# Performance work log

Measured on AMD Instinct MI355X. Metric: run time of the kernel, lower is better.

## Reference

```python
import jax, jax.numpy as jnp
import numpy as np

EMBED_DIM = 1024
NUM_HEADS = 16
SEQ_LEN = 2048
BATCH = 2
LN_EPS = 1e-5


def setup_inputs() -> dict:
    key = jax.random.key(0)
    ks = jax.random.split(key, 12)
    d = EMBED_DIM
    s = 1.0 / np.sqrt(d)
    inp = {
        "x": jax.random.normal(ks[0], (BATCH, SEQ_LEN, d), dtype=jnp.float32),
        "ln1_g": jnp.ones((d,), jnp.float32),
        "ln1_b": jnp.zeros((d,), jnp.float32),
        "ln2_g": jnp.ones((d,), jnp.float32),
        "ln2_b": jnp.zeros((d,), jnp.float32),
        "W_qkv": jax.random.normal(ks[1], (d, 3 * d), jnp.float32) * s,
        "b_qkv": jnp.zeros((3 * d,), jnp.float32),
        "W_proj": jax.random.normal(ks[2], (d, d), jnp.float32) * s,
        "b_proj": jnp.zeros((d,), jnp.float32),
        "W_fc": jax.random.normal(ks[3], (d, 4 * d), jnp.float32) * s,
        "b_fc": jnp.zeros((4 * d,), jnp.float32),
        "W_out": jax.random.normal(ks[4], (4 * d, d), jnpp_dummy := jnp.float32) * (1.0 / np.sqrt(4 * d)),
        "b_out": jnp.zeros((d,), jnp.float32),
    }
    return inp


def _layernorm(x, g, b):
    mu = jnp.mean(x, axis=-1, keepdims=True)
    var = jnp.mean(jnp.square(x - mu), axis=-1, keepdims=True)
    return (x - mu) * jax.lax.rsqrt(var + LN_EPS) * g + b


def _block(x, ln1_g, ln1_b, ln2_g, ln2_b, W_qkv, b_qkv, W_proj, b_proj, W_fc, b_fc, W_out, b_out):
    B, S, D = x.shape
    H = NUM_HEADS
    hd = D // H
    h = _layernorm(x, ln1_g, ln1_b)
    qkv = h @ W_qkv + b_qkv  # [B,S,3D]
    q, k, v = jnp.split(qkv, 3, axis=-1)
    # [B,H,S,hd]
    q = q.reshape(B, S, H, hd).transpose(0, 2, 1, 3)
    k = k.reshape(B, S, H, hd).transpose(0, 2, 1, 3)
    v = v.reshape(B, S, H, hd).transpose(0, 2, 1, 3)
    attn = jnp.einsum("bhqd,bhkd->bhqk", q, k) / np.sqrt(hd).astype(np.float32)
    causal = jnp.tril(jnp.ones((S, S), dtype=bool))
    attn = jnp.where(causal, attn, -jnp.inf)
    attn = jax.nn.softmax(attn, axis=-1)
    y = jnp.einsum("bhqk,bhkd->bhqd", attn, v)
    y = y.transpose(0, 2, 1, 3).reshape(B, S, D)
    y = y @ W_proj + b_proj
    x = x + y
    h2 = _layernorm(x, ln2_g, ln2_b)
    m = jax.nn.relu(h2 @ W_fc + b_fc) @ W_out + b_out
    return x + m


def reference(x, ln1_g, ln1_b, ln2_g, ln2_b, W_qkv, b_qkv, W_proj, b_proj, W_fc, b_fc, W_out, b_out):
    return _block(x, ln1_g, ln1_b, ln2_g, ln2_b, W_qkv, b_qkv, W_proj, b_proj, W_fc, b_fc, W_out, b_out)
```

## Files before the change

kernel.cpp:

```cpp
#include <hip/hip_runtime.h>

typedef unsigned short u16;
typedef __attribute__((ext_vector_type(8))) __bf16 bf16x8;
typedef __attribute__((ext_vector_type(4))) float f32x4;

#define DEV __device__ __forceinline__

DEV u16 f2bf(float f) {
  unsigned u = __float_as_uint(f);
  u += 0x7fffu + ((u >> 16) & 1u);
  return (u16)(u >> 16);
}
DEV float bf2f(u16 u) { return __uint_as_float((unsigned)u << 16); }

DEV void gl_lds16(const void* g, void* l) {
  __builtin_amdgcn_global_load_lds(
      (const __attribute__((address_space(1))) void*)(uintptr_t)g,
      (__attribute__((address_space(3))) void*)(unsigned)(uintptr_t)l, 16, 0, 0);
}

DEV float wave_sum64(float v) {
#pragma unroll
  for (int off = 32; off > 0; off >>= 1) v += __shfl_down(v, off);
  return v;
}

DEV void ln_body(const float4 v, const float* g, const float* be, u16* out_row, int t,
                 float* red) {
  const int w = t >> 6, L = t & 63;
  float s = v.x + v.y + v.z + v.w;
  s = wave_sum64(s);
  if (L == 0) red[w] = s;
  __syncthreads();
  const float mean = (red[0] + red[1] + red[2] + red[3]) * (1.0f / 1024.0f);
  const float dx = v.x - mean, dy = v.y - mean, dz = v.z - mean, dw = v.w - mean;
  float q = dx * dx + dy * dy + dz * dz + dw * dw;
  q = wave_sum64(q);
  if (L == 0) red[4 + w] = q;
  __syncthreads();
  const float var = (red[4] + red[5] + red[6] + red[7]) * (1.0f / 1024.0f);
  const float rs = rsqrtf(var + 1e-5f);
  const float4 gg = reinterpret_cast<const float4*>(g)[t];
  const float4 bb = reinterpret_cast<const float4*>(be)[t];
  ushort4 o;
  o.x = f2bf(dx * rs * gg.x + bb.x);
  o.y = f2bf(dy * rs * gg.y + bb.y);
  o.z = f2bf(dz * rs * gg.z + bb.z);
  o.w = f2bf(dw * rs * gg.w + bb.w);
  reinterpret_cast<ushort4*>(out_row)[t] = o;
}

__global__ __launch_bounds__(256) void prep_kernel(
    const float* __restrict__ x, const float* __restrict__ ln1g,
    const float* __restrict__ ln1b, u16* __restrict__ hbuf,
    const float* __restrict__ Wqkv, u16* __restrict__ wt_qkv,
    const float* __restrict__ Wproj, u16* __restrict__ wt_proj,
    const float* __restrict__ Wfc, u16* __restrict__ wt_fc,
    const float* __restrict__ Wout, u16* __restrict__ wt_out) {
  __shared__ float smem[32 * 33];
  int id = blockIdx.x;
  const int t = threadIdx.x;
  if (id < 4096) {
    const float4 v = reinterpret_cast<const float4*>(x + (size_t)id * 1024)[t];
    ln_body(v, ln1g, ln1b, hbuf + (size_t)id * 1024, t, smem);
    return;
  }
  id -= 4096;
  const float* W;
  u16* Wt;
  int K, N, nbx;
  if (id < 3072) {
    W = Wqkv; Wt = wt_qkv; K = 1024; N = 3072; nbx = 96;
  } else if (id < 3072 + 1024) {
    id -= 3072; W = Wproj; Wt = wt_proj; K = 1024; N = 1024; nbx = 32;
  } else if (id < 3072 + 1024 + 4096) {
    id -= 3072 + 1024; W = Wfc; Wt = wt_fc; K = 1024; N = 4096; nbx = 128;
  } else {
    id -= 3072 + 1024 + 4096; W = Wout; Wt = wt_out; K = 4096; N = 1024; nbx = 32;
  }
  float(*tile)[33] = (float(*)[33])smem;
  const int c0 = (id % nbx) * 32, r0 = (id / nbx) * 32;
  const int tx = t & 31, ty = t >> 5;
#pragma unroll
  for (int j = 0; j < 4; ++j)
    tile[ty + j * 8][tx] = W[(size_t)(r0 + ty + j * 8) * N + c0 + tx];
  __syncthreads();
#pragma unroll
  for (int j = 0; j < 4; ++j) {
    const int n = c0 + ty + j * 8, k = r0 + tx;
    Wt[(size_t)n * K + k] = f2bf(tile[tx][ty + j * 8]);
  }
}

__global__ __launch_bounds__(256) void proj_reduce_ln(const float* __restrict__ x,
                                                      const float* __restrict__ bias,
                                                      const u16* __restrict__ P0,
                                                      const u16* __restrict__ P1,
                                                      const float* __restrict__ g,
                                                      const float* __restrict__ be,
                                                      float* __restrict__ x2,
                                                      u16* __restrict__ hbuf) {
  const int row = blockIdx.x, t = threadIdx.x;
  const size_t off = (size_t)row * 1024;
  __shared__ float red[8];
  const float4 xv = reinterpret_cast<const float4*>(x + off)[t];
  const float4 bv = reinterpret_cast<const float4*>(bias)[t];
  const ushort4 p0 = reinterpret_cast<const ushort4*>(P0 + off)[t];
  const ushort4 p1 = reinterpret_cast<const ushort4*>(P1 + off)[t];
  float4 v;
  v.x = xv.x + bv.x + bf2f(p0.x) + bf2f(p1.x);
  v.y = xv.y + bv.y + bf2f(p0.y) + bf2f(p1.y);
  v.z = xv.z + bv.z + bf2f(p0.z) + bf2f(p1.z);
  v.w = xv.w + bv.w + bf2f(p0.w) + bf2f(p1.w);
  reinterpret_cast<float4*>(x2 + off)[t] = v;
  ln_body(v, g, be, hbuf + off, t, red);
}

__global__ __launch_bounds__(256) void out_reduce(const float* __restrict__ x2,
                                                  const float* __restrict__ bias,
                                                  const u16* __restrict__ P0,
                                                  const u16* __restrict__ P1,
                                                  const u16* __restrict__ P2,
                                                  const u16* __restrict__ P3,
                                                  float* __restrict__ dout) {
  const int row = blockIdx.x, t = threadIdx.x;
  const size_t off = (size_t)row * 1024;
  const float4 xv = reinterpret_cast<const float4*>(x2 + off)[t];
  const float4 bv = reinterpret_cast<const float4*>(bias)[t];
  const ushort4 a = reinterpret_cast<const ushort4*>(P0 + off)[t];
  const ushort4 b = reinterpret_cast<const ushort4*>(P1 + off)[t];
  const ushort4 c = reinterpret_cast<const ushort4*>(P2 + off)[t];
  const ushort4 d = reinterpret_cast<const ushort4*>(P3 + off)[t];
  float4 o;
  o.x = xv.x + bv.x + bf2f(a.x) + bf2f(b.x) + bf2f(c.x) + bf2f(d.x);
  o.y = xv.y + bv.y + bf2f(a.y) + bf2f(b.y) + bf2f(c.y) + bf2f(d.y);
  o.z = xv.z + bv.z + bf2f(a.z) + bf2f(b.z) + bf2f(c.z) + bf2f(d.z);
  o.w = xv.w + bv.w + bf2f(a.w) + bf2f(b.w) + bf2f(c.w) + bf2f(d.w);
  reinterpret_cast<float4*>(dout + off)[t] = o;
}

enum { F_BIAS = 1, F_RESID = 2, F_RELU = 4, F_BF16 = 8, F_PART4 = 32, F_VT = 64 };

template <int FLAGS>
__global__ __launch_bounds__(256, 2) void gemm_bt(const u16* __restrict__ A,
                                                  const u16* __restrict__ Bt,
                                                  const float* __restrict__ bias,
                                                  const float* __restrict__ resid,
                                                  void* __restrict__ Cout,
                                                  u16* __restrict__ pp0, u16* __restrict__ pp1,
                                                  u16* __restrict__ pp2, u16* __restrict__ pp3,
                                                  int M, int N, int K, int Kst) {
  __shared__ __attribute__((aligned(16))) u16 sA[2][128 * 32];
  __shared__ __attribute__((aligned(16))) u16 sB[2][128 * 32];

  const int gx = gridDim.x, gy = gridDim.y;
  const int tilesPerZ = gx * gy;
  int lin = (blockIdx.z * gy + blockIdx.y) * gx + blockIdx.x;
  const int total = tilesPerZ * gridDim.z;
  if (!(total & 7)) lin = (lin & 7) * (total >> 3) + (lin >> 3);
  const int zz = lin / tilesPerZ;
  const int pid = lin - zz * tilesPerZ;
  const int npg = gx << 3;
  const int gid = pid / npg;
  const int rem = pid - gid * npg;
  const int fm = gid << 3;
  const int gsm = (gy - fm < 8) ? (gy - fm) : 8;
  const int bm = fm + rem % gsm;
  const int bn = rem / gsm;

  const int t = threadIdx.x, w = t >> 6, L = t & 63, quad = L >> 4, l15 = L & 15;
  const int wm = w >> 1, wn = w & 1;
  const int m0 = bm * 128, n0 = bn * 128;
  const u16* Ag = A + (size_t)m0 * Kst + (size_t)zz * K;
  const u16* Bg = Bt + (size_t)n0 * Kst + (size_t)zz * K;

  f32x4 acc[4][4] = {};

  for (int k0 = 0; k0 < K; k0 += 64) {
    __syncthreads();
#pragma unroll
    for (int h = 0; h < 2; ++h) {
#pragma unroll
      for (int i = 0; i < 2; ++i) {
        const int cp = i * 256 + t, rr = cp >> 2, cc = (cp & 3) << 3;
        gl_lds16(Ag + (size_t)rr * Kst + k0 + h * 32 + cc, &sA[h][(i * 256 + w * 64) * 8]);
      }
#pragma unroll
      for (int i = 0; i < 2; ++i) {
        const int cp = i * 256 + t, rr = cp >> 2, cc = (cp & 3) << 3;
        gl_lds16(Bg + (size_t)rr * Kst + k0 + h * 32 + cc, &sB[h][(i * 256 + w * 64) * 8]);
      }
    }
    __syncthreads();

#pragma unroll
    for (int h = 0; h < 2; ++h) {
      bf16x8 af[4], bfr[4];
#pragma unroll
      for (int m = 0; m < 4; ++m)
        af[m] = *(const bf16x8*)&sA[h][(wm * 64 + m * 16 + l15) * 32 + quad * 8];
#pragma unroll
      for (int n = 0; n < 4; ++n)
        bfr[n] = *(const bf16x8*)&sB[h][(wn * 64 + n * 16 + l15) * 32 + quad * 8];
#pragma unroll
      for (int m = 0; m < 4; ++m)
#pragma unroll
        for (int n = 0; n < 4; ++n)
          acc[m][n] =
              __builtin_amdgcn_mfma_f32_16x16x32_bf16(af[m], bfr[n], acc[m][n], 0, 0, 0);
    }
  }

  if ((FLAGS & F_VT) && n0 >= 2048) {
#pragma unroll
    for (int m = 0; m < 4; ++m) {
#pragma unroll
      for (int n = 0; n < 4; ++n) {
        const int col = n0 + wn * 64 + n * 16 + l15;
        const float bv = bias[col];
        const int hh = (col - 2048) >> 6, dd = col & 63;
        const int srow = m0 + wm * 64 + m * 16 + quad * 4;
        const int bb = srow >> 11, ss = srow & 2047;
        ushort4 tmp;
        tmp.x = f2bf(acc[m][n][0] + bv);
        tmp.y = f2bf(acc[m][n][1] + bv);
        tmp.z = f2bf(acc[m][n][2] + bv);
        tmp.w = f2bf(acc[m][n][3] + bv);
        *(ushort4*)(pp0 + ((size_t)((bb * 16 + hh) * 64 + dd)) * 2048 + ss) = tmp;
      }
    }
    return;
  }

  u16* pbase = nullptr;
  if (FLAGS & F_PART4)
    pbase = (zz == 0) ? pp0 : (zz == 1) ? pp1 : (zz == 2) ? pp2 : pp3;

#pragma unroll
  for (int m = 0; m < 4; ++m) {
#pragma unroll
    for (int n = 0; n < 4; ++n) {
      const int col = n0 + wn * 64 + n * 16 + l15;
      const float bv = (FLAGS & F_BIAS) ? bias[col] : 0.0f;
#pragma unroll
      for (int rr = 0; rr < 4; ++rr) {
        const int row = m0 + wm * 64 + m * 16 + quad * 4 + rr;
        if (FLAGS & F_PART4) {
          pbase[(size_t)row * N + col] = f2bf(acc[m][n][rr]);
        } else {
          float v = acc[m][n][rr] + bv;
          if (FLAGS & F_RESID) v += resid[(size_t)row * N + col];
          if (FLAGS & F_RELU) v = fmaxf(v, 0.0f);
          if (FLAGS & F_BF16)
            ((u16*)Cout)[(size_t)row * N + col] = f2bf(v);
          else
            ((float*)Cout)[(size_t)row * N + col] = v;
        }
      }
    }
  }
}

__global__ __launch_bounds__(256) void flash_attn(const u16* __restrict__ qkv,
                                                  const u16* __restrict__ Vt,
                                                  u16* __restrict__ y) {
  constexpr int S = 2048, D3 = 3072, D = 1024;
  constexpr float Csc = 0.125f * 1.44269504088896f;
  __shared__ __attribute__((aligned(16))) u16 sK[2 * 64 * 32];
  __shared__ __attribute__((aligned(16))) u16 sV[2 * 64 * 32];
  __shared__ __attribute__((aligned(16))) u16 sP[4][2 * 16 * 40];

  const int lin = blockIdx.x;
  const int half = lin >> 9, rem = lin & 511;
  const int qt = half ? (31 - (rem & 31)) : (rem & 31);
  const int bh = (rem >> 5) | (half << 4);
  const int b = bh >> 4, h = bh & 15;
  const int q0 = qt * 64;

  const int t = threadIdx.x, w = t >> 6, L = t & 63, quad = L >> 4, l15 = L & 15;
  const int qw = q0 + w * 16;

  const u16* qbase = qkv + (size_t)(b * S) * D3 + h * 64;
  const u16* Kbase = qbase + D;
  const u16* Vbase = Vt + (size_t)((b * 16 + h) * 64) * S;

  bf16x8 aQ[2];
#pragma unroll
  for (int kk = 0; kk < 2; ++kk)
    aQ[kk] = *(const bf16x8*)(qbase + (size_t)(qw + l15) * D3 + kk * 32 + quad * 8);

  bf16x8 ones;
#pragma unroll
  for (int i = 0; i < 8; ++i) ones[i] = (__bf16)1.0f;

  f32x4 acc[4] = {};
  f32x4 lacc = {};

  u16* sPw = sP[w];
  const int nkv = qt + 1;
  for (int it = 0; it < nkv; ++it) {
    const int kv0 = it * 64;
    __syncthreads();
#pragma unroll
    for (int i = 0; i < 2; ++i) {
      const int cp = i * 256 + t;
      const int kk = cp >> 8, r = (cp >> 2) & 63, col = (cp & 3) << 3;
      gl_lds16(Kbase + (size_t)(kv0 + r) * D3 + kk * 32 + col, &sK[(i * 256 + w * 64) * 8]);
    }
#pragma unroll
    for (int i = 0; i < 2; ++i) {
      const int cp = i * 256 + t;
      const int kk = cp >> 8, d = (cp >> 2) & 63, col = (cp & 3) << 3;
      gl_lds16(Vbase + (size_t)d * S + kv0 + kk * 32 + col, &sV[(i * 256 + w * 64) * 8]);
    }
    __syncthreads();

    f32x4 s[4] = {};
#pragma unroll
    for (int kk = 0; kk < 2; ++kk) {
#pragma unroll
      for (int n = 0; n < 4; ++n) {
        const bf16x8 bK = *(const bf16x8*)&sK[kk * 2048 + (n * 16 + l15) * 32 + quad * 8];
        s[n] = __builtin_amdgcn_mfma_f32_16x16x32_bf16(aQ[kk], bK, s[n], 0, 0, 0);
      }
    }

    if (kv0 + 63 > qw) {
#pragma unroll
      for (int n = 0; n < 4; ++n) {
        const int col = kv0 + n * 16 + l15;
#pragma unroll
        for (int r = 0; r < 4; ++r) {
          const int row = qw + quad * 4 + r;
          const float p = __builtin_amdgcn_exp2f(s[n][r] * Csc);
          s[n][r] = (col > row) ? 0.0f : p;
        }
      }
    } else {
#pragma unroll
      for (int n = 0; n < 4; ++n)
#pragma unroll
        for (int r = 0; r < 4; ++r) s[n][r] = __builtin_amdgcn_exp2f(s[n][r] * Csc);
    }

#pragma unroll
    for (int n = 0; n < 4; ++n)
#pragma unroll
      for (int r = 0; r < 4; ++r)
        sPw[(n >> 1) * 640 + (quad * 4 + r) * 40 + (n & 1) * 16 + l15] = f2bf(s[n][r]);

#pragma unroll
    for (int kk = 0; kk < 2; ++kk) {
      const bf16x8 aP = *(const bf16x8*)&sPw[kk * 640 + l15 * 40 + quad * 8];
      lacc = __builtin_amdgcn_mfma_f32_16x16x32_bf16(aP, ones, lacc, 0, 0, 0);
#pragma unroll
      for (int dn = 0; dn < 4; ++dn) {
        const bf16x8 bV = *(const bf16x8*)&sV[kk * 2048 + (dn * 16 + l15) * 32 + quad * 8];
        acc[dn] = __builtin_amdgcn_mfma_f32_16x16x32_bf16(aP, bV, acc[dn], 0, 0, 0);
      }
    }
  }

#pragma unroll
  for (int r = 0; r < 4; ++r) {
    const float inv = 1.0f / lacc[r];
    const int row = qw + quad * 4 + r;
    u16* yb = y + (size_t)(b * S + row) * D + h * 64 + l15;
#pragma unroll
    for (int dn = 0; dn < 4; ++dn) yb[dn * 16] = f2bf(acc[dn][r] * inv);
  }
}

extern "C" void kernel_launch(void* const* d_in, const int* in_sizes, int n_in,
                              void* d_out, int out_size, void* d_ws, size_t ws_size,
                              hipStream_t stream) {
  const float* x = (const float*)d_in[0];
  const float* ln1g = (const float*)d_in[1];
  const float* ln1b = (const float*)d_in[2];
  const float* ln2g = (const float*)d_in[3];
  const float* ln2b = (const float*)d_in[4];
  const float* Wqkv = (const float*)d_in[5];
  const float* bqkv = (const float*)d_in[6];
  const float* Wproj = (const float*)d_in[7];
  const float* bproj = (const float*)d_in[8];
  const float* Wfc = (const float*)d_in[9];
  const float* bfc = (const float*)d_in[10];
  const float* Wout = (const float*)d_in[11];
  const float* bout = (const float*)d_in[12];

  char* ws = (char*)d_ws;
  const size_t MB = 1u << 20;
  u16* wt_out = (u16*)(ws + 0 * MB);
  u16* hbuf = (u16*)(ws + 8 * MB);
  float* x2 = (float*)(ws + 16 * MB);
  u16* ybuf = (u16*)(ws + 32 * MB);
  u16* qkvb = (u16*)(ws + 40 * MB);
  u16* vtb = (u16*)(ws + 64 * MB);
  u16* wt_qkv = (u16*)(ws + 72 * MB);
  u16* wt_proj = (u16*)(ws + 78 * MB);
  u16* wt_fc = (u16*)(ws + 80 * MB);
  u16* projP0 = (u16*)(ws + 40 * MB);
  u16* projP1 = (u16*)(ws + 48 * MB);
  u16* m1 = (u16*)(ws + 40 * MB);
  u16* po0 = (u16*)(ws + 8 * MB);
  u16* po1 = (u16*)(ws + 32 * MB);
  u16* po2 = (u16*)(ws + 72 * MB);
  u16* po3 = (u16*)(ws + 80 * MB);

  prep_kernel<<<4096 + 3072 + 1024 + 4096 + 4096, 256, 0, stream>>>(
      x, ln1g, ln1b, hbuf, Wqkv, wt_qkv, Wproj, wt_proj, Wfc, wt_fc, Wout, wt_out);

  gemm_bt<F_BIAS | F_BF16 | F_VT><<<dim3(24, 32), 256, 0, stream>>>(
      hbuf, wt_qkv, bqkv, nullptr, qkvb, vtb, nullptr, nullptr, nullptr,
      4096, 3072, 1024, 1024);
  flash_attn<<<1024, 256, 0, stream>>>(qkvb, vtb, ybuf);

  gemm_bt<F_PART4><<<dim3(8, 32, 2), 256, 0, stream>>>(
      ybuf, wt_proj, nullptr, nullptr, nullptr, projP0, projP1, nullptr, nullptr,
      4096, 1024, 512, 1024);
  proj_reduce_ln<<<4096, 256, 0, stream>>>(x, bproj, projP0, projP1, ln2g, ln2b, x2, hbuf);

  gemm_bt<F_BIAS | F_RELU | F_BF16><<<dim3(32, 32), 256, 0, stream>>>(
      hbuf, wt_fc, bfc, nullptr, m1, nullptr, nullptr, nullptr, nullptr,
      4096, 4096, 1024, 1024);

  gemm_bt<F_PART4><<<dim3(8, 32, 4), 256, 0, stream>>>(
      m1, wt_out, nullptr, nullptr, nullptr, po0, po1, po2, po3,
      4096, 1024, 1024, 4096);
  out_reduce<<<4096, 256, 0, stream>>>(x2, bout, po0, po1, po2, po3, (float*)d_out);
}
```

Measured before the change: 320.8 us.

## Double-buffer K/V tiles in flash attention with XOR-swizzled LDS layout

```diff
diff --git a/kernel.cpp b/kernel.cpp
--- a/kernel.cpp
+++ b/kernel.cpp
@@ -266,8 +266,8 @@
                                                   u16* __restrict__ y) {
   constexpr int S = 2048, D3 = 3072, D = 1024;
   constexpr float Csc = 0.125f * 1.44269504088896f;
-  __shared__ __attribute__((aligned(16))) u16 sK[2 * 64 * 32];
-  __shared__ __attribute__((aligned(16))) u16 sV[2 * 64 * 32];
+  __shared__ __attribute__((aligned(16))) u16 sK[2][64 * 64];
+  __shared__ __attribute__((aligned(16))) u16 sV[2][64 * 64];
   __shared__ __attribute__((aligned(16))) u16 sP[4][2 * 16 * 40];
 
   const int lin = blockIdx.x;
@@ -284,6 +284,17 @@
   const u16* Kbase = qbase + D;
   const u16* Vbase = Vt + (size_t)((b * 16 + h) * 64) * S;
 
+  const u16* Ksrc[2];
+  const u16* Vsrc[2];
+#pragma unroll
+  for (int i = 0; i < 2; ++i) {
+    const int p = i * 256 + t;
+    const int row = p >> 3;
+    const int k8 = ((p & 7) ^ (row & 7)) << 3;
+    Ksrc[i] = Kbase + (size_t)row * D3 + k8;
+    Vsrc[i] = Vbase + (size_t)row * S + k8;
+  }
+
   bf16x8 aQ[2];
 #pragma unroll
   for (int kk = 0; kk < 2; ++kk)
@@ -297,30 +308,43 @@
   f32x4 lacc = {};
 
   u16* sPw = sP[w];
+  const int swz = l15 & 7;
   const int nkv = qt + 1;
+
+#pragma unroll
+  for (int i = 0; i < 2; ++i)
+    gl_lds16(Ksrc[i], &sK[0][(i * 256 + w * 64) * 8]);
+#pragma unroll
+  for (int i = 0; i < 2; ++i)
+    gl_lds16(Vsrc[i], &sV[0][(i * 256 + w * 64) * 8]);
+
+  int cur = 0;
   for (int it = 0; it < nkv; ++it) {
     const int kv0 = it * 64;
-    __syncthreads();
-#pragma unroll
-    for (int i = 0; i < 2; ++i) {
-      const int cp = i * 256 + t;
-      const int kk = cp >> 8, r = (cp >> 2) & 63, col = (cp & 3) << 3;
-      gl_lds16(Kbase + (size_t)(kv0 + r) * D3 + kk * 32 + col, &sK[(i * 256 + w * 64) * 8]);
-    }
-#pragma unroll
-    for (int i = 0; i < 2; ++i) {
-      const int cp = i * 256 + t;
-      const int kk = cp >> 8, d = (cp >> 2) & 63, col = (cp & 3) << 3;
-      gl_lds16(Vbase + (size_t)d * S + kv0 + kk * 32 + col, &sV[(i * 256 + w * 64) * 8]);
-    }
-    __syncthreads();
+    if (it + 1 < nkv) {
+      const int kvn = kv0 + 64;
+#pragma unroll
+      for (int i = 0; i < 2; ++i)
+        gl_lds16(Ksrc[i] + (size_t)kvn * D3, &sK[cur ^ 1][(i * 256 + w * 64) * 8]);
+#pragma unroll
+      for (int i = 0; i < 2; ++i)
+        gl_lds16(Vsrc[i] + kvn, &sV[cur ^ 1][(i * 256 + w * 64) * 8]);
+      asm volatile("s_waitcnt vmcnt(4)" ::: "memory");
+    } else {
+      asm volatile("s_waitcnt vmcnt(0)" ::: "memory");
+    }
+    __builtin_amdgcn_s_barrier();
+
+    const u16* sKc = sK[cur];
+    const u16* sVc = sV[cur];
 
     f32x4 s[4] = {};
 #pragma unroll
     for (int kk = 0; kk < 2; ++kk) {
 #pragma unroll
       for (int n = 0; n < 4; ++n) {
-        const bf16x8 bK = *(const bf16x8*)&sK[kk * 2048 + (n * 16 + l15) * 32 + quad * 8];
+        const bf16x8 bK =
+            *(const bf16x8*)&sKc[(n * 16 + l15) * 64 + ((kk * 4 + quad) ^ swz) * 8];
         s[n] = __builtin_amdgcn_mfma_f32_16x16x32_bf16(aQ[kk], bK, s[n], 0, 0, 0);
       }
     }
@@ -355,10 +379,15 @@
       lacc = __builtin_amdgcn_mfma_f32_16x16x32_bf16(aP, ones, lacc, 0, 0, 0);
 #pragma unroll
       for (int dn = 0; dn < 4; ++dn) {
-        const bf16x8 bV = *(const bf16x8*)&sV[kk * 2048 + (dn * 16 + l15) * 32 + quad * 8];
+        const bf16x8 bV =
+            *(const bf16x8*)&sVc[(dn * 16 + l15) * 64 + ((kk * 4 + quad) ^ swz) * 8];
         acc[dn] = __builtin_amdgcn_mfma_f32_16x16x32_bf16(aP, bV, acc[dn], 0, 0, 0);
       }
     }
+
+    asm volatile("s_waitcnt lgkmcnt(0)" ::: "memory");
+    __builtin_amdgcn_s_barrier();
+    cur ^= 1;
   }
 
 #pragma unroll
```

Result: no change. 323.9 us (+1.0%).
